# Performance work log

Measured on AMD Instinct MI355X. Metric: run time of the kernel, lower is better.

Reference implementation:

```python
import jax, jax.numpy as jnp
import numpy as np

NUM_PARTS = 16
NUM_K = 256          # num_k_per_part; table rows per part = NUM_K + 1
VAE_DIMS = 768
OUT_DIMS = 1024
B = 4096


def setup_inputs() -> dict:
    key = jax.random.key(0)
    k0, k1, k2, k3, k4 = jax.random.split(key, 5)
    hashes = jax.random.randint(k0, (B, NUM_PARTS), 0, NUM_K + 1)  # values 0..256
    # nn.init.normal_(embedding.weight, 0.0, 0.01)
    emb = jax.random.normal(k1, ((NUM_K + 1) * NUM_PARTS, VAE_DIMS), dtype=jnp.float32) * 0.01
    # projection: Linear(768 -> 1024), ReLU, Linear(1024 -> 1024)
    W1 = jax.random.normal(k2, (VAE_DIMS, OUT_DIMS), dtype=jnp.float32) * (1.0 / np.sqrt(VAE_DIMS))
    b1 = jnp.zeros((OUT_DIMS,), dtype=jnp.float32)
    W2 = jax.random.normal(k3, (OUT_DIMS, OUT_DIMS), dtype=jnp.float32) * (1.0 / np.sqrt(OUT_DIMS))
    b2 = jnp.zeros((OUT_DIMS,), dtype=jnp.float32)
    # pe = randn(num_parts, out_dims) * 1.0
    pe = jax.random.normal(k4, (NUM_PARTS, OUT_DIMS), dtype=jnp.float32)
    return {"hashes": hashes, "emb": emb, "W1": W1, "b1": b1, "W2": W2, "b2": b2, "pe": pe}


def reference(hashes, emb, W1, b1, W2, b2, pe):
    # forward(hashes, index=None, get_mu=False, input_is_mu=False)
    offset = jnp.arange(NUM_PARTS, dtype=hashes.dtype) * (NUM_K + 1)  # [P]
    idx = hashes + offset[None, :]                                    # [B, P]
    mu = emb[idx]                                                     # [B, P, VAE]
    h = jax.nn.relu(jnp.einsum('bpv,vh->bph', mu, W1) + b1)           # [B, P, OUT]
    projected = jnp.einsum('bph,ho->bpo', h, W2) + b2                 # [B, P, OUT]
    return projected + pe[None, :, :]                                 # pe broadcast over batch
```

## Files before the change

kernel.cpp:

```cpp
#include <hip/hip_runtime.h>
#include <stdint.h>

#define NPARTS 16
#define NK1    257
#define ROWS   4112
#define MPAD   4224
#define VAE    768
#define ODIM   1024
#define BROWS  65536

typedef __attribute__((ext_vector_type(4))) float f32x4;
typedef __attribute__((ext_vector_type(8))) short s16x8;

static __device__ __forceinline__ unsigned short f2bf(float f) {
  union { float f; unsigned u; } v; v.f = f;
  unsigned x = v.u;
  unsigned r = x + 0x7FFFu + ((x >> 16) & 1u);
  return (unsigned short)(r >> 16);
}

static __device__ __forceinline__ void gload_lds16(const void* g, void* l) {
  __builtin_amdgcn_global_load_lds(
      (const __attribute__((address_space(1))) unsigned int*)g,
      (__attribute__((address_space(3))) unsigned int*)l, 16, 0, 0);
}

#define EMB_BLOCKS 1024
__global__ __launch_bounds__(256) void prep_kernel(
    const float* __restrict__ emb, const float* __restrict__ W1,
    unsigned short* __restrict__ embB, unsigned short* __restrict__ w1t) {
  __shared__ unsigned short tile[32][33];
  const int tid = threadIdx.x;
  const int bid = blockIdx.x;
  if (bid < EMB_BLOCKS) {
    const int NQ = MPAD * VAE / 4;
    for (int g = bid * 256 + tid; g < NQ; g += EMB_BLOCKS * 256) {
      const int i4 = g * 4;
      ushort4 o;
      if (i4 < ROWS * VAE) {
        const float4 v = *(const float4*)(emb + i4);
        o.x = f2bf(v.x); o.y = f2bf(v.y); o.z = f2bf(v.z); o.w = f2bf(v.w);
      } else {
        o.x = 0; o.y = 0; o.z = 0; o.w = 0;
      }
      *(ushort4*)(embB + i4) = o;
    }
  } else {
    const int tb = bid - EMB_BLOCKS;
    const int nkt = VAE / 32;
    const int tk = (tb % nkt) * 32;
    const int tn = (tb / nkt) * 32;
    const int r  = tid >> 3;
    const int c4 = (tid & 7) * 4;
    const float4 v = *(const float4*)(W1 + (size_t)(tk + r) * ODIM + tn + c4);
    tile[r][c4 + 0] = f2bf(v.x);
    tile[r][c4 + 1] = f2bf(v.y);
    tile[r][c4 + 2] = f2bf(v.z);
    tile[r][c4 + 3] = f2bf(v.w);
    __syncthreads();
    ushort4 o;
    o.x = tile[c4 + 0][r];
    o.y = tile[c4 + 1][r];
    o.z = tile[c4 + 2][r];
    o.w = tile[c4 + 3][r];
    *(ushort4*)(w1t + (size_t)(tn + r) * VAE + tk + c4) = o;
  }
}

template <int K, int MODE, bool DO_W2T>
__global__ __launch_bounds__(256) void gemm_kernel(
    const unsigned short* __restrict__ A, const unsigned short* __restrict__ BT,
    const float* __restrict__ bias, const float* __restrict__ pe,
    unsigned short* __restrict__ outB, float* __restrict__ outF,
    const float* __restrict__ W2src, unsigned short* __restrict__ w2dst) {
  __shared__ __align__(16) unsigned short smem[3 * 12288];
  const int tid = threadIdx.x;

  if (DO_W2T && blockIdx.z == 1) {
    if (blockIdx.y >= 32) return;
    unsigned short (*ttile)[132] = (unsigned short (*)[132])smem;
    const int tk = blockIdx.y * 32, tn = blockIdx.x * 128;
#pragma unroll
    for (int q = 0; q < 4; ++q) {
      const int row = (tid >> 5) + q * 8, c4 = (tid & 31) * 4;
      const float4 v = *(const float4*)(W2src + (size_t)(tk + row) * ODIM + tn + c4);
      ttile[row][c4 + 0] = f2bf(v.x); ttile[row][c4 + 1] = f2bf(v.y);
      ttile[row][c4 + 2] = f2bf(v.z); ttile[row][c4 + 3] = f2bf(v.w);
    }
    __syncthreads();
#pragma unroll
    for (int q = 0; q < 4; ++q) {
      const int n = (tid >> 3) + q * 32, k4 = (tid & 7) * 4;
      ushort4 o;
      o.x = ttile[k4 + 0][n]; o.y = ttile[k4 + 1][n];
      o.z = ttile[k4 + 2][n]; o.w = ttile[k4 + 3][n];
      *(ushort4*)(w2dst + (size_t)(tn + n) * ODIM + tk + k4) = o;
    }
    return;
  }

  const int lane = tid & 63;
  const int wave = tid >> 6;
  const int wc   = wave * 32;
  const int brow = blockIdx.y * 64;
  const int bcol = blockIdx.x * 128;
  const int la   = lane & 15;
  const int hi   = lane >> 4;

  f32x4 acc[4][2];
#pragma unroll
  for (int m = 0; m < 4; ++m)
#pragma unroll
    for (int n = 0; n < 2; ++n)
#pragma unroll
      for (int r = 0; r < 4; ++r) acc[m][n][r] = 0.f;

  const int srow = tid >> 3;
  const int skb  = (tid & 7) ^ (srow & 7);
  const unsigned short* gA = A + (size_t)(brow + srow) * K + skb * 8;
  const unsigned short* gB = BT + (size_t)(bcol + srow) * K + skb * 8;

#define STAGE(b, kt)                                              \
  {                                                               \
    unsigned short* la_ = smem + (b) * 12288 + tid * 8;           \
    unsigned short* lb_ = la_ + 4096;                             \
    gload_lds16(gA + (kt), la_);                                  \
    gload_lds16(gA + (kt) + 32 * K, la_ + 2048);                  \
    gload_lds16(gB + (kt), lb_);                                  \
    gload_lds16(gB + (kt) + 32 * K, lb_ + 2048);                  \
    gload_lds16(gB + (kt) + 64 * K, lb_ + 4096);                  \
    gload_lds16(gB + (kt) + 96 * K, lb_ + 6144);                  \
  }

  const int NT = K / 64;
  STAGE(0, 0);
  STAGE(1, 64);

#pragma unroll
  for (int t = 0; t < NT; ++t) {
    if (t < NT - 1) asm volatile("s_waitcnt vmcnt(6)" ::: "memory");
    else            asm volatile("s_waitcnt vmcnt(0)" ::: "memory");
    __builtin_amdgcn_sched_barrier(0);
    __builtin_amdgcn_s_barrier();
    if (t + 2 < NT) STAGE((t + 2) % 3, (t + 2) * 64);

    const unsigned short* As = smem + (t % 3) * 12288;
    const unsigned short* Bs = As + 4096;
    s16x8 af[4][2], bf[2][2];
#pragma unroll
    for (int m = 0; m < 4; ++m)
#pragma unroll
      for (int ks = 0; ks < 2; ++ks)
        af[m][ks] = *(const s16x8*)(As + (m * 16 + la) * 64 +
                                    (((ks * 4 + hi) ^ (la & 7)) * 8));
#pragma unroll
    for (int n = 0; n < 2; ++n)
#pragma unroll
      for (int ks = 0; ks < 2; ++ks)
        bf[n][ks] = *(const s16x8*)(Bs + (wc + n * 16 + la) * 64 +
                                    (((ks * 4 + hi) ^ (la & 7)) * 8));
    asm volatile("s_waitcnt lgkmcnt(0)" ::: "memory");
    __builtin_amdgcn_sched_barrier(0);

    __builtin_amdgcn_s_setprio(1);
#pragma unroll
    for (int m = 0; m < 4; ++m)
#pragma unroll
      for (int n = 0; n < 2; ++n)
#pragma unroll
        for (int ks = 0; ks < 2; ++ks)
          acc[m][n] = __builtin_amdgcn_mfma_f32_16x16x32_bf16(af[m][ks], bf[n][ks],
                                                              acc[m][n], 0, 0, 0);
    __builtin_amdgcn_s_setprio(0);
  }
#undef STAGE

#pragma unroll
  for (int m = 0; m < 4; ++m) {
    const int row0 = brow + m * 16 + hi * 4;
#pragma unroll
    for (int n = 0; n < 2; ++n) {
      const int col = bcol + wc + n * 16 + la;
      const float bv = bias[col];
      if (MODE == 0) {
#pragma unroll
        for (int r = 0; r < 4; ++r) {
          float v = acc[m][n][r] + bv;
          v = v > 0.f ? v : 0.f;
          outB[(size_t)(row0 + r) * ODIM + col] = f2bf(v);
        }
      } else {
#pragma unroll
        for (int r = 0; r < 4; ++r) {
          const int row = row0 + r;
          int p = row / NK1;
          if (p > NPARTS - 1) p = NPARTS - 1;
          outF[(size_t)row * ODIM + col] = acc[m][n][r] + bv + pe[(size_t)p * ODIM + col];
        }
      }
    }
  }
}

__global__ __launch_bounds__(256) void gather_kernel(const int* __restrict__ hashes,
                                                     const float* __restrict__ T,
                                                     float* __restrict__ out) {
  const int wid  = (blockIdx.x * blockDim.x + threadIdx.x) >> 6;
  const int lane = threadIdx.x & 63;
  const int nw   = (gridDim.x * blockDim.x) >> 6;
  for (int row = wid; row < BROWS; row += nw) {
    const int h = __builtin_amdgcn_readfirstlane(hashes[row]);
    const int p = row & (NPARTS - 1);
    const f32x4* __restrict__ src = (const f32x4*)(T + (size_t)(h + p * NK1) * ODIM);
    f32x4* __restrict__ dst = (f32x4*)(out + (size_t)row * ODIM);
#pragma unroll
    for (int j = 0; j < 4; ++j) {
      f32x4 v = src[lane + j * 64];
      __builtin_nontemporal_store(v, dst + lane + j * 64);
    }
  }
}

extern "C" void kernel_launch(void* const* d_in, const int* in_sizes, int n_in,
                              void* d_out, int out_size, void* d_ws, size_t ws_size,
                              hipStream_t stream) {
  const int*   hashes = (const int*)d_in[0];
  const float* emb    = (const float*)d_in[1];
  const float* W1     = (const float*)d_in[2];
  const float* b1     = (const float*)d_in[3];
  const float* W2     = (const float*)d_in[4];
  const float* b2     = (const float*)d_in[5];
  const float* pe     = (const float*)d_in[6];
  float* out = (float*)d_out;

  char* ws = (char*)d_ws;
  unsigned short* embB = (unsigned short*)(ws);
  unsigned short* w1t  = (unsigned short*)(ws + 6488064);
  unsigned short* w2t  = (unsigned short*)(ws + 8060928);
  unsigned short* H    = (unsigned short*)(ws + 10158080);
  float*          T    = (float*)(ws + 18808832);

  prep_kernel<<<EMB_BLOCKS + 768, 256, 0, stream>>>(emb, W1, embB, w1t);

  gemm_kernel<VAE, 0, true><<<dim3(8, 66, 2), 256, 0, stream>>>(
      embB, w1t, b1, nullptr, H, nullptr, W2, w2t);

  gemm_kernel<ODIM, 2, false><<<dim3(8, 66, 1), 256, 0, stream>>>(
      H, w2t, b2, pe, nullptr, T, nullptr, nullptr);

  gather_kernel<<<2048, 256, 0, stream>>>(hashes, T, out);
}
```

Measured before the change: 95.36 us.

## Enlarge GEMM tiles to 128x128 with 2x2 wave layout and double buffering

Changes the GEMM block tile from 64x128 to 128x128, with each wave computing a 64x64 sub-tile (4x4 MFMA accumulators) instead of 64x32. This raises reuse of the LDS fragments per MFMA and halves the grid rows. The pipeline also changes from a 3-stage buffer with explicit vmcnt waits and setprio to a simpler 2-stage double buffer with __syncthreads. The W2 transpose path still only uses blockIdx.y<32, so with 33 rows the transpose coverage is unchanged. The cost is fewer blocks (264 per GEMM, about one wave of blocks on 256 CUs), more registers, and weaker load/compute overlap.

```diff
diff --git a/kernel.cpp b/kernel.cpp
--- a/kernel.cpp
+++ b/kernel.cpp
@@ -73,7 +73,7 @@
     const float* __restrict__ bias, const float* __restrict__ pe,
     unsigned short* __restrict__ outB, float* __restrict__ outF,
     const float* __restrict__ W2src, unsigned short* __restrict__ w2dst) {
-  __shared__ __align__(16) unsigned short smem[3 * 12288];
+  __shared__ __align__(16) unsigned short smem[2 * 16384];
   const int tid = threadIdx.x;
 
   if (DO_W2T && blockIdx.z == 1) {
@@ -101,17 +101,18 @@
 
   const int lane = tid & 63;
   const int wave = tid >> 6;
-  const int wc   = wave * 32;
-  const int brow = blockIdx.y * 64;
+  const int wr   = (wave >> 1) * 64;
+  const int wc   = (wave & 1) * 64;
+  const int brow = blockIdx.y * 128;
   const int bcol = blockIdx.x * 128;
   const int la   = lane & 15;
   const int hi   = lane >> 4;
 
-  f32x4 acc[4][2];
+  f32x4 acc[4][4];
 #pragma unroll
   for (int m = 0; m < 4; ++m)
 #pragma unroll
-    for (int n = 0; n < 2; ++n)
+    for (int n = 0; n < 4; ++n)
 #pragma unroll
       for (int r = 0; r < 4; ++r) acc[m][n][r] = 0.f;
 
@@ -122,64 +123,55 @@
 
 #define STAGE(b, kt)                                              \
   {                                                               \
-    unsigned short* la_ = smem + (b) * 12288 + tid * 8;           \
-    unsigned short* lb_ = la_ + 4096;                             \
+    unsigned short* la_ = smem + (b) * 16384 + tid * 8;           \
+    unsigned short* lb_ = la_ + 8192;                             \
     gload_lds16(gA + (kt), la_);                                  \
     gload_lds16(gA + (kt) + 32 * K, la_ + 2048);                  \
+    gload_lds16(gA + (kt) + 64 * K, la_ + 4096);                  \
+    gload_lds16(gA + (kt) + 96 * K, la_ + 6144);                  \
     gload_lds16(gB + (kt), lb_);                                  \
     gload_lds16(gB + (kt) + 32 * K, lb_ + 2048);                  \
     gload_lds16(gB + (kt) + 64 * K, lb_ + 4096);                  \
     gload_lds16(gB + (kt) + 96 * K, lb_ + 6144);                  \
   }
 
+  STAGE(0, 0);
+  __syncthreads();
+
   const int NT = K / 64;
-  STAGE(0, 0);
-  STAGE(1, 64);
-
-#pragma unroll
   for (int t = 0; t < NT; ++t) {
-    if (t < NT - 1) asm volatile("s_waitcnt vmcnt(6)" ::: "memory");
-    else            asm volatile("s_waitcnt vmcnt(0)" ::: "memory");
-    __builtin_amdgcn_sched_barrier(0);
-    __builtin_amdgcn_s_barrier();
-    if (t + 2 < NT) STAGE((t + 2) % 3, (t + 2) * 64);
-
-    const unsigned short* As = smem + (t % 3) * 12288;
-    const unsigned short* Bs = As + 4096;
-    s16x8 af[4][2], bf[2][2];
-#pragma unroll
-    for (int m = 0; m < 4; ++m)
-#pragma unroll
-      for (int ks = 0; ks < 2; ++ks)
-        af[m][ks] = *(const s16x8*)(As + (m * 16 + la) * 64 +
-                                    (((ks * 4 + hi) ^ (la & 7)) * 8));
-#pragma unroll
-    for (int n = 0; n < 2; ++n)
-#pragma unroll
-      for (int ks = 0; ks < 2; ++ks)
-        bf[n][ks] = *(const s16x8*)(Bs + (wc + n * 16 + la) * 64 +
-                                    (((ks * 4 + hi) ^ (la & 7)) * 8));
-    asm volatile("s_waitcnt lgkmcnt(0)" ::: "memory");
-    __builtin_amdgcn_sched_barrier(0);
-
-    __builtin_amdgcn_s_setprio(1);
-#pragma unroll
-    for (int m = 0; m < 4; ++m)
-#pragma unroll
-      for (int n = 0; n < 2; ++n)
-#pragma unroll
-        for (int ks = 0; ks < 2; ++ks)
-          acc[m][n] = __builtin_amdgcn_mfma_f32_16x16x32_bf16(af[m][ks], bf[n][ks],
+    const int cur = t & 1;
+    if (t + 1 < NT) STAGE(cur ^ 1, (t + 1) * 64);
+
+    const unsigned short* As = smem + cur * 16384;
+    const unsigned short* Bs = As + 8192;
+#pragma unroll
+    for (int ks = 0; ks < 2; ++ks) {
+      s16x8 af[4], bf[4];
+#pragma unroll
+      for (int m = 0; m < 4; ++m)
+        af[m] = *(const s16x8*)(As + (wr + m * 16 + la) * 64 +
+                                (((ks * 4 + hi) ^ (la & 7)) * 8));
+#pragma unroll
+      for (int n = 0; n < 4; ++n)
+        bf[n] = *(const s16x8*)(Bs + (wc + n * 16 + la) * 64 +
+                                (((ks * 4 + hi) ^ (la & 7)) * 8));
+#pragma unroll
+      for (int m = 0; m < 4; ++m)
+#pragma unroll
+        for (int n = 0; n < 4; ++n)
+          acc[m][n] = __builtin_amdgcn_mfma_f32_16x16x32_bf16(af[m], bf[n],
                                                               acc[m][n], 0, 0, 0);
-    __builtin_amdgcn_s_setprio(0);
+    }
+    __syncthreads();
   }
 #undef STAGE
 
 #pragma unroll
   for (int m = 0; m < 4; ++m) {
-    const int row0 = brow + m * 16 + hi * 4;
-#pragma unroll
-    for (int n = 0; n < 2; ++n) {
+    const int row0 = brow + wr + m * 16 + hi * 4;
+#pragma unroll
+    for (int n = 0; n < 4; ++n) {
       const int col = bcol + wc + n * 16 + la;
       const float bv = bias[col];
       if (MODE == 0) {
@@ -242,10 +234,10 @@
 
   prep_kernel<<<EMB_BLOCKS + 768, 256, 0, stream>>>(emb, W1, embB, w1t);
 
-  gemm_kernel<VAE, 0, true><<<dim3(8, 66, 2), 256, 0, stream>>>(
+  gemm_kernel<VAE, 0, true><<<dim3(8, 33, 2), 256, 0, stream>>>(
       embB, w1t, b1, nullptr, H, nullptr, W2, w2t);
 
-  gemm_kernel<ODIM, 2, false><<<dim3(8, 66, 1), 256, 0, stream>>>(
+  gemm_kernel<ODIM, 2, false><<<dim3(8, 33, 1), 256, 0, stream>>>(
       H, w2t, b2, pe, nullptr, T, nullptr, nullptr);
 
   gather_kernel<<<2048, 256, 0, stream>>>(hashes, T, out);
```

Result: slower. 97.55 us (+2.3%).
